# Performance work log

Hardware: AMD Instinct MI355X
Metric: run time of the kernel (lower is better)

The kernel has to match this reference:

```python
import jax, jax.numpy as jnp
import numpy as np

N_EMBD = 1024
N_HEAD = 16
HEAD_SIZE = N_EMBD // N_HEAD


def setup_inputs() -> dict:
    key = jax.random.key(0)
    k_x, k_w, k_b = jax.random.split(key, 3)
    B, T, C = 2, 2048, N_EMBD
    x = jax.random.normal(k_x, (B, T, C), dtype=jnp.float32)
    # Linear(n_embd, 3*n_embd): weight [C, 3C] (applied as x @ W), bias [3C]
    w_qkv = jax.random.normal(k_w, (C, 3 * C), dtype=jnp.float32) * (1.0 / np.sqrt(C))
    b_qkv = jax.random.normal(k_b, (3 * C,), dtype=jnp.float32) * 0.02
    return {"x": x, "w_qkv": w_qkv, "b_qkv": b_qkv}


def reference(x, w_qkv, b_qkv):
    B, T, C = x.shape
    H, D = N_HEAD, HEAD_SIZE
    qkv = x @ w_qkv + b_qkv                      # [B, T, 3C]
    q, k, v = jnp.split(qkv, 3, axis=-1)         # each [B, T, C]
    # [B, T, C] -> [B, H, T, D]
    q = q.reshape(B, T, H, D).transpose(0, 2, 1, 3)
    k = k.reshape(B, T, H, D).transpose(0, 2, 1, 3)
    v = v.reshape(B, T, H, D).transpose(0, 2, 1, 3)
    scores = jnp.einsum('bhqd,bhkd->bhqk', q, k) / jnp.sqrt(jnp.float32(D))
    causal = jnp.tril(jnp.ones((T, T), dtype=bool))  # allow j <= i
    scores = jnp.where(causal[None, None, :, :], scores, -jnp.inf)
    weights = jax.nn.softmax(scores, axis=-1)    # [B, H, T, T]
    out = jnp.einsum('bhqk,bhkd->bhqd', weights, v)
    out = out.transpose(0, 2, 1, 3).reshape(B, T, C)
    return out
```

## Files before the change

### kernel.cpp

```cpp
#include <hip/hip_runtime.h>
#include <hip/hip_bf16.h>


#define CDIM  1024
#define C3    3072
#define HS    64
#define TLEN  2048
#define KVT   64
#define KSTR  72
#define VSTR  72
#define SCL   0.1803368801111204f

typedef __attribute__((ext_vector_type(8))) short bf16x8;
typedef __attribute__((ext_vector_type(4))) float f32x4;
typedef __attribute__((ext_vector_type(4))) unsigned short u16x4;

__device__ __forceinline__ unsigned short f2b(float f) {
    unsigned u = __float_as_uint(f);
    unsigned r = (u + 0x7FFFu + ((u >> 16) & 1u)) >> 16;
    return (unsigned short)r;
}
__device__ __forceinline__ float b2f(unsigned short u) {
    return __uint_as_float(((unsigned)u) << 16);
}
__device__ __forceinline__ float fexp2(float x) {
    return __builtin_amdgcn_exp2f(x);
}
__device__ __forceinline__ unsigned pkbf(float a, float b) {
    float2 f; f.x = a; f.y = b;
    __hip_bfloat162 h = __float22bfloat162_rn(f);
    union { __hip_bfloat162 h2; unsigned u; } c;
    c.h2 = h;
    return c.u;
}
__device__ __forceinline__ void gl_lds16(const unsigned short* g, unsigned short* l) {
    __builtin_amdgcn_global_load_lds((const __attribute__((address_space(1))) void*)g,
                                     (__attribute__((address_space(3))) void*)l, 16, 0, 0);
}
__device__ __forceinline__ int detect_bf(const void* bias, int lane) {
    unsigned w = ((const unsigned*)bias)[lane];
    unsigned e = (w >> 7) & 0xFF;
    unsigned long long m = __ballot(e >= 100 && e <= 135);
    return __popcll(m) >= 48;
}

__device__ __forceinline__ void plswap(unsigned x, unsigned& y0, unsigned& y1) {
    unsigned aa = x, bb = x;
    asm("v_permlane32_swap_b32 %0, %1" : "+v"(aa), "+v"(bb));
    asm("v_permlane16_swap_b32 %0, %1" : "+v"(aa), "+v"(bb));
    y0 = aa; y1 = bb;
}
__device__ __forceinline__ bf16x8 xfrag(unsigned x00, unsigned x01,
                                        unsigned x10, unsigned x11, int qsel) {
    unsigned y000, y100, y001, y101, y010, y110, y011, y111;
    plswap(x00, y000, y100);
    plswap(x01, y001, y101);
    plswap(x10, y010, y110);
    plswap(x11, y011, y111);
    union { unsigned u[4]; bf16x8 v; } r;
    r.u[0] = qsel ? y010 : y000;
    r.u[1] = qsel ? y011 : y001;
    r.u[2] = qsel ? y110 : y100;
    r.u[3] = qsel ? y111 : y101;
    return r.v;
}

__global__ __launch_bounds__(256) void k_prep(const void* __restrict__ w,
                                              const void* __restrict__ x,
                                              const void* __restrict__ bias,
                                              unsigned short* __restrict__ wt,
                                              unsigned short* __restrict__ xb) {
    __shared__ unsigned short tile[64 * 66];
    int t = threadIdx.x;
    int isbf = detect_bf(bias, t & 63);
    int bid = blockIdx.x;

    if (bid < 768) {
        int n0 = (bid % 48) * 64;
        int k0 = (bid / 48) * 64;
        for (int i = 0; i < 16; ++i) {
            int idx = t + i * 256;
            int r = idx >> 6, c = idx & 63;
            unsigned short v;
            if (isbf) v = ((const unsigned short*)w)[(k0 + r) * C3 + n0 + c];
            else      v = f2b(((const float*)w)[(k0 + r) * C3 + n0 + c]);
            tile[r * 66 + c] = v;
        }
        __syncthreads();
        for (int i = 0; i < 16; ++i) {
            int idx = t + i * 256;
            int r = idx >> 6, c = idx & 63;
            wt[(n0 + r) * CDIM + k0 + c] = tile[c * 66 + r];
        }
    }
    if (!isbf) {
        const float* s = (const float*)x;
        unsigned* d = (unsigned*)xb;
        int base = bid * 1024;
        for (int j = t; j < 1024; j += 256) {
            int idx = base + j;
            float a = s[2 * idx], b = s[2 * idx + 1];
            d[idx] = (unsigned)f2b(a) | ((unsigned)f2b(b) << 16);
        }
    }
}

__global__ __launch_bounds__(256, 3) void k_gemm_qkv(const void* __restrict__ xraw,
                                                     const unsigned short* __restrict__ xb,
                                                     const void* __restrict__ biasraw,
                                                     const unsigned short* __restrict__ Bt,
                                                     unsigned short* __restrict__ qk,
                                                     unsigned short* __restrict__ vtg) {
    __shared__ __align__(16) unsigned short As[128 * 64];
    __shared__ __align__(16) unsigned short Bs[128 * 64];
    int tid  = threadIdx.x;
    int lane = tid & 63, wv = tid >> 6;
    int quad = lane >> 4, l16 = lane & 15;
    int isbf = detect_bf(biasraw, lane);
    const unsigned short* A = isbf ? (const unsigned short*)xraw : xb;

    int lin = blockIdx.x + 24 * blockIdx.y;
    int swz = (lin & 7) * 96 + (lin >> 3);
    int m0 = (swz / 24) * 128, n0 = (swz % 24) * 128;
    int wm = (wv >> 1) * 64, wn = (wv & 1) * 64;

    f32x4 acc[4][4] = {};

    int srow = wv * 8 + (lane >> 3);
    int kcg8 = (((lane & 7) ^ (lane >> 3)) * 8);
    const unsigned short* Ag = A  + (m0 + srow) * CDIM + kcg8;
    const unsigned short* Bg = Bt + (n0 + srow) * CDIM + kcg8;
    unsigned short* lA = &As[srow * 64 + (lane & 7) * 8];
    unsigned short* lB = &Bs[srow * 64 + (lane & 7) * 8];

    for (int k0 = 0; k0 < CDIM; k0 += 64) {
        __syncthreads();
        for (int j = 0; j < 4; ++j) {
            gl_lds16(Ag + j * (32 * CDIM), lA + j * (32 * 64));
            gl_lds16(Bg + j * (32 * CDIM), lB + j * (32 * 64));
        }
        Ag += 64; Bg += 64;
        __syncthreads();

        for (int kk = 0; kk < 2; ++kk) {
            int sw = (l16 & 7);
            bf16x8 af[4], bfr[4];
            for (int mt = 0; mt < 4; ++mt)
                af[mt] = *(const bf16x8*)&As[(wm + mt * 16 + l16) * 64 + (((kk * 4 + quad) ^ sw) * 8)];
            for (int nt = 0; nt < 4; ++nt)
                bfr[nt] = *(const bf16x8*)&Bs[(wn + nt * 16 + l16) * 64 + (((kk * 4 + quad) ^ sw) * 8)];
            for (int mt = 0; mt < 4; ++mt)
                for (int nt = 0; nt < 4; ++nt)
                    acc[mt][nt] = __builtin_amdgcn_mfma_f32_16x16x32_bf16(af[mt], bfr[nt], acc[mt][nt], 0, 0, 0);
        }
    }

    if (n0 < 2048) {
        for (int mt = 0; mt < 4; ++mt) {
            int row = m0 + wm + mt * 16 + quad * 4;
            for (int nt = 0; nt < 4; ++nt) {
                int col = n0 + wn + nt * 16 + l16;
                float bv = isbf ? b2f(((const unsigned short*)biasraw)[col])
                                : ((const float*)biasraw)[col];
                for (int i = 0; i < 4; ++i)
                    qk[(row + i) * 2048 + col] = f2b(acc[mt][nt][i] + bv);
            }
        }
    } else {
        for (int mt = 0; mt < 4; ++mt) {
            int row = m0 + wm + mt * 16 + quad * 4;
            int t = row & 2047, b = row >> 11;
            for (int nt = 0; nt < 4; ++nt) {
                int col = n0 + wn + nt * 16 + l16;
                float bv = isbf ? b2f(((const unsigned short*)biasraw)[col])
                                : ((const float*)biasraw)[col];
                int hh = (col - 2048) >> 6, d = (col - 2048) & 63;
                u16x4 pk;
                for (int i = 0; i < 4; ++i) pk[i] = f2b(acc[mt][nt][i] + bv);
                *(u16x4*)&vtg[((b * 16 + hh) * 64 + d) * TLEN + t] = pk;
            }
        }
    }
}

__global__ __launch_bounds__(256, 4) void k_attn(const unsigned short* __restrict__ qk,
                                                 const unsigned short* __restrict__ vtg,
                                                 const void* __restrict__ biasraw,
                                                 void* __restrict__ outv) {
    __shared__ __align__(16) unsigned short SM[2 * 64 * KSTR];
    unsigned short* Ks = SM;
    unsigned short* Vt = SM + 64 * KSTR;

    int tid  = threadIdx.x;
    int lane = tid & 63, wv = tid >> 6;
    int quad = lane >> 4, l16 = lane & 15;
    int isbf = detect_bf(biasraw, lane);
    int bh = blockIdx.x;
    int g  = 31 - blockIdx.y;
    int b = bh >> 4, h = bh & 15;
    int rowbase = b * TLEN;

    int s_ = wv >> 1;
    int p  = wv & 1;
    int qbase = 64 * g + 32 * s_;
    int T = g + 1;

    bf16x8 qf[2][2];
    for (int qt = 0; qt < 2; ++qt)
        for (int kh = 0; kh < 2; ++kh)
            qf[qt][kh] = *(const bf16x8*)&qk[(rowbase + qbase + qt * 16 + l16) * 2048
                                            + h * HS + kh * 32 + quad * 8];

    f32x4 o[2][4] = {};
    float ls[2] = {0.f, 0.f};

    int srow = tid >> 2;
    int sc   = (tid & 3) * 8;
    const unsigned short* kgB = qk  + (rowbase + srow) * 2048 + CDIM + h * HS + sc;
    const unsigned short* vgB = vtg + (bh * 64 + srow) * TLEN + sc;

    {
        uint4 k0 = *(const uint4*)kgB;
        uint4 k1 = *(const uint4*)(kgB + 32);
        uint4 v0 = *(const uint4*)vgB;
        uint4 v1 = *(const uint4*)(vgB + 32);
        *(uint4*)&Ks[srow * KSTR + sc]      = k0;
        *(uint4*)&Ks[srow * KSTR + sc + 32] = k1;
        *(uint4*)&Vt[srow * VSTR + sc]      = v0;
        *(uint4*)&Vt[srow * VSTR + sc + 32] = v1;
    }
    const unsigned short* kpf = kgB + KVT * 2048;
    const unsigned short* vpf = vgB + KVT;
    __syncthreads();

    for (int t = 0; t < T; ++t) {
        int kv0 = t * KVT;
        bool act = (p == 0) || (s_ == 1) || (t < T - 1);
        bool dm  = (t == T - 1) && (p == s_);

        uint4 kn0, kn1, vn0, vn1;
        bool pf = (t + 1 < T);
        if (pf) {
            kn0 = *(const uint4*)kpf;
            kn1 = *(const uint4*)(kpf + 32);
            vn0 = *(const uint4*)vpf;
            vn1 = *(const uint4*)(vpf + 32);
            kpf += KVT * 2048;
            vpf += KVT;
        }

        unsigned sp[2][2][2];
        if (act) {
            bf16x8 kf[2][2];
            #pragma unroll
            for (int nt = 0; nt < 2; ++nt) {
                const unsigned short* kb = &Ks[(32 * p + nt * 16 + l16) * KSTR + quad * 8];
                kf[nt][0] = *(const bf16x8*)kb;
                kf[nt][1] = *(const bf16x8*)(kb + 32);
            }
            f32x4 sv[2][2];
            __builtin_amdgcn_s_setprio(1);
            #pragma unroll
            for (int qt = 0; qt < 2; ++qt)
                #pragma unroll
                for (int nt = 0; nt < 2; ++nt) {
                    f32x4 z = {};
                    z = __builtin_amdgcn_mfma_f32_16x16x32_bf16(kf[nt][0], qf[qt][0], z, 0, 0, 0);
                    z = __builtin_amdgcn_mfma_f32_16x16x32_bf16(kf[nt][1], qf[qt][1], z, 0, 0, 0);
                    sv[qt][nt] = z;
                }
            __builtin_amdgcn_s_setprio(0);
            #pragma unroll
            for (int qt = 0; qt < 2; ++qt) {
                float psum = 0.f;
                int q = qbase + qt * 16 + l16;
                #pragma unroll
                for (int nt = 0; nt < 2; ++nt) {
                    float pv[4];
                    #pragma unroll
                    for (int i = 0; i < 4; ++i) {
                        float arg = fminf(fmaf(sv[qt][nt][i], SCL, -12.0f), 30.0f);
                        if (dm) {
                            int kv = kv0 + 32 * p + nt * 16 + quad * 4 + i;
                            if (kv > q) arg = -1e30f;
                        }
                        pv[i] = fexp2(arg);
                        psum += pv[i];
                    }
                    sp[qt][nt][0] = pkbf(pv[0], pv[1]);
                    sp[qt][nt][1] = pkbf(pv[2], pv[3]);
                }
                ls[qt] += psum;
            }
            int qsel = quad & 2;
            bf16x8 f0 = xfrag(sp[0][0][0], sp[0][0][1], sp[0][1][0], sp[0][1][1], qsel);
            bf16x8 f1 = xfrag(sp[1][0][0], sp[1][0][1], sp[1][1][0], sp[1][1][1], qsel);
            __builtin_amdgcn_s_setprio(1);
            #pragma unroll
            for (int dt = 0; dt < 4; ++dt) {
                bf16x8 av = *(const bf16x8*)&Vt[(dt * 16 + l16) * VSTR + 32 * p + quad * 8];
                o[0][dt] = __builtin_amdgcn_mfma_f32_16x16x32_bf16(av, f0, o[0][dt], 0, 0, 0);
                o[1][dt] = __builtin_amdgcn_mfma_f32_16x16x32_bf16(av, f1, o[1][dt], 0, 0, 0);
            }
            __builtin_amdgcn_s_setprio(0);
        }

        __syncthreads();
        if (pf) {
            *(uint4*)&Ks[srow * KSTR + sc]      = kn0;
            *(uint4*)&Ks[srow * KSTR + sc + 32] = kn1;
            *(uint4*)&Vt[srow * VSTR + sc]      = vn0;
            *(uint4*)&Vt[srow * VSTR + sc + 32] = vn1;
        }
        __syncthreads();
    }

    #pragma unroll
    for (int qt = 0; qt < 2; ++qt) {
        ls[qt] += __shfl_xor(ls[qt], 16);
        ls[qt] += __shfl_xor(ls[qt], 32);
    }
    float* mrg  = (float*)SM;
    float* lbuf = (float*)SM + 4352;

    if (p == 1) {
        #pragma unroll
        for (int qt = 0; qt < 2; ++qt)
            #pragma unroll
            for (int dt = 0; dt < 4; ++dt)
                *(f32x4*)&mrg[s_ * (32 * 68) + (qt * 16 + l16) * 68 + dt * 16 + quad * 4] = o[qt][dt];
        if (quad == 0) {
            lbuf[s_ * 32 + l16]      = ls[0];
            lbuf[s_ * 32 + 16 + l16] = ls[1];
        }
    }
    __syncthreads();
    if (p == 0) {
        #pragma unroll
        for (int qt = 0; qt < 2; ++qt) {
            float lt = ls[qt] + lbuf[s_ * 32 + qt * 16 + l16];
            float inv = 1.0f / lt;
            int q = qbase + qt * 16 + l16;
            if (isbf) {
                unsigned short* out = (unsigned short*)outv;
                #pragma unroll
                for (int dt = 0; dt < 4; ++dt) {
                    f32x4 m = *(const f32x4*)&mrg[s_ * (32 * 68) + (qt * 16 + l16) * 68 + dt * 16 + quad * 4];
                    u16x4 ov;
                    #pragma unroll
                    for (int i = 0; i < 4; ++i) ov[i] = f2b((o[qt][dt][i] + m[i]) * inv);
                    *(u16x4*)&out[(rowbase + q) * CDIM + h * HS + dt * 16 + quad * 4] = ov;
                }
            } else {
                float* out = (float*)outv;
                #pragma unroll
                for (int dt = 0; dt < 4; ++dt) {
                    f32x4 m = *(const f32x4*)&mrg[s_ * (32 * 68) + (qt * 16 + l16) * 68 + dt * 16 + quad * 4];
                    float4 ov;
                    ov.x = (o[qt][dt][0] + m[0]) * inv;
                    ov.y = (o[qt][dt][1] + m[1]) * inv;
                    ov.z = (o[qt][dt][2] + m[2]) * inv;
                    ov.w = (o[qt][dt][3] + m[3]) * inv;
                    *(float4*)&out[(rowbase + q) * CDIM + h * HS + dt * 16 + quad * 4] = ov;
                }
            }
        }
    }
}

extern "C" void kernel_launch(void* const* d_in, const int* in_sizes, int n_in,
                              void* d_out, int out_size, void* d_ws, size_t ws_size,
                              hipStream_t stream) {
    const void* x    = d_in[0];
    const void* w    = d_in[1];
    const void* bias = d_in[2];

    char* ws = (char*)d_ws;
    unsigned short* xb  = (unsigned short*)ws;
    unsigned short* wt  = (unsigned short*)(ws + (8u  << 20));
    unsigned short* qk  = (unsigned short*)(ws + (16u << 20));
    unsigned short* vtg = (unsigned short*)(ws + (32u << 20));

    k_prep<<<2048, 256, 0, stream>>>(w, x, bias, wt, xb);
    k_gemm_qkv<<<dim3(24, 32), 256, 0, stream>>>(x, xb, bias, wt, qk, vtg);
    k_attn<<<dim3(32, 32), 256, 0, stream>>>(qk, vtg, bias, d_out);
}
```

Baseline: 150.6 us.

## Load K/V fragments directly from global into registers, drop LDS staging and barriers

The attention kernel no longer stages K and V tiles through shared memory with two block barriers per iteration. Each wave now loads its own MFMA K and V^T fragments straight from global memory into registers, with a one-tile register prefetch for K. Waves with no work on the final tile get a shorter loop, and the causal-mask branch is split out so the common path skips the mask test. The trade is losing cross-wave data sharing: K/V reads are replicated per wave, and the global accesses are uncoalesced and rely on cache hits, in exchange for removing the barrier stalls.

```diff
diff --git a/kernel.cpp b/kernel.cpp
--- a/kernel.cpp
+++ b/kernel.cpp
@@ -7,8 +7,6 @@
 #define HS    64
 #define TLEN  2048
 #define KVT   64
-#define KSTR  72
-#define VSTR  72
 #define SCL   0.1803368801111204f
 
 typedef __attribute__((ext_vector_type(8))) short bf16x8;
@@ -187,9 +185,7 @@
                                                  const unsigned short* __restrict__ vtg,
                                                  const void* __restrict__ biasraw,
                                                  void* __restrict__ outv) {
-    __shared__ __align__(16) unsigned short SM[2 * 64 * KSTR];
-    unsigned short* Ks = SM;
-    unsigned short* Vt = SM + 64 * KSTR;
+    __shared__ __align__(16) float SMf[4416];
 
     int tid  = threadIdx.x;
     int lane = tid & 63, wv = tid >> 6;
@@ -203,7 +199,9 @@
     int s_ = wv >> 1;
     int p  = wv & 1;
     int qbase = 64 * g + 32 * s_;
-    int T = g + 1;
+    int T  = g + 1;
+    int Tw = T - ((s_ == 0 && p == 1) ? 1 : 0);
+    bool dmw = (p == s_);
 
     bf16x8 qf[2][2];
     for (int qt = 0; qt < 2; ++qt)
@@ -214,62 +212,54 @@
     f32x4 o[2][4] = {};
     float ls[2] = {0.f, 0.f};
 
-    int srow = tid >> 2;
-    int sc   = (tid & 3) * 8;
-    const unsigned short* kgB = qk  + (rowbase + srow) * 2048 + CDIM + h * HS + sc;
-    const unsigned short* vgB = vtg + (bh * 64 + srow) * TLEN + sc;
-
-    {
-        uint4 k0 = *(const uint4*)kgB;
-        uint4 k1 = *(const uint4*)(kgB + 32);
-        uint4 v0 = *(const uint4*)vgB;
-        uint4 v1 = *(const uint4*)(vgB + 32);
-        *(uint4*)&Ks[srow * KSTR + sc]      = k0;
-        *(uint4*)&Ks[srow * KSTR + sc + 32] = k1;
-        *(uint4*)&Vt[srow * VSTR + sc]      = v0;
-        *(uint4*)&Vt[srow * VSTR + sc + 32] = v1;
-    }
-    const unsigned short* kpf = kgB + KVT * 2048;
-    const unsigned short* vpf = vgB + KVT;
-    __syncthreads();
-
-    for (int t = 0; t < T; ++t) {
-        int kv0 = t * KVT;
-        bool act = (p == 0) || (s_ == 1) || (t < T - 1);
-        bool dm  = (t == T - 1) && (p == s_);
-
-        uint4 kn0, kn1, vn0, vn1;
-        bool pf = (t + 1 < T);
+    const unsigned short* kp0 = qk + (rowbase + 32 * p + l16) * 2048 + CDIM + h * HS + quad * 8;
+    const unsigned short* kp1 = kp0 + 16 * 2048;
+    const unsigned short* vpb = vtg + (bh * 64 + l16) * 2048 + 32 * p + quad * 8;
+    const unsigned short* vp0 = vpb;
+    const unsigned short* vp1 = vpb + 16 * 2048;
+    const unsigned short* vp2 = vpb + 32 * 2048;
+    const unsigned short* vp3 = vpb + 48 * 2048;
+
+    bf16x8 kA00, kA01, kA10, kA11;
+    if (Tw > 0) {
+        kA00 = *(const bf16x8*)kp0; kA01 = *(const bf16x8*)(kp0 + 32);
+        kA10 = *(const bf16x8*)kp1; kA11 = *(const bf16x8*)(kp1 + 32);
+        kp0 += KVT * 2048; kp1 += KVT * 2048;
+    }
+
+    for (int t = 0; t < Tw; ++t) {
+        bf16x8 av0 = *(const bf16x8*)vp0;
+        bf16x8 av1 = *(const bf16x8*)vp1;
+        bf16x8 av2 = *(const bf16x8*)vp2;
+        bf16x8 av3 = *(const bf16x8*)vp3;
+        vp0 += KVT; vp1 += KVT; vp2 += KVT; vp3 += KVT;
+
+        f32x4 sv[2][2];
+        __builtin_amdgcn_s_setprio(1);
+        #pragma unroll
+        for (int qt = 0; qt < 2; ++qt) {
+            f32x4 z0 = {};
+            z0 = __builtin_amdgcn_mfma_f32_16x16x32_bf16(kA00, qf[qt][0], z0, 0, 0, 0);
+            z0 = __builtin_amdgcn_mfma_f32_16x16x32_bf16(kA01, qf[qt][1], z0, 0, 0, 0);
+            sv[qt][0] = z0;
+            f32x4 z1 = {};
+            z1 = __builtin_amdgcn_mfma_f32_16x16x32_bf16(kA10, qf[qt][0], z1, 0, 0, 0);
+            z1 = __builtin_amdgcn_mfma_f32_16x16x32_bf16(kA11, qf[qt][1], z1, 0, 0, 0);
+            sv[qt][1] = z1;
+        }
+        __builtin_amdgcn_s_setprio(0);
+
+        bf16x8 kB00, kB01, kB10, kB11;
+        bool pf = (t + 1 < Tw);
         if (pf) {
-            kn0 = *(const uint4*)kpf;
-            kn1 = *(const uint4*)(kpf + 32);
-            vn0 = *(const uint4*)vpf;
-            vn1 = *(const uint4*)(vpf + 32);
-            kpf += KVT * 2048;
-            vpf += KVT;
+            kB00 = *(const bf16x8*)kp0; kB01 = *(const bf16x8*)(kp0 + 32);
+            kB10 = *(const bf16x8*)kp1; kB11 = *(const bf16x8*)(kp1 + 32);
+            kp0 += KVT * 2048; kp1 += KVT * 2048;
         }
 
         unsigned sp[2][2][2];
-        if (act) {
-            bf16x8 kf[2][2];
-            #pragma unroll
-            for (int nt = 0; nt < 2; ++nt) {
-                const unsigned short* kb = &Ks[(32 * p + nt * 16 + l16) * KSTR + quad * 8];
-                kf[nt][0] = *(const bf16x8*)kb;
-                kf[nt][1] = *(const bf16x8*)(kb + 32);
-            }
-            f32x4 sv[2][2];
-            __builtin_amdgcn_s_setprio(1);
-            #pragma unroll
-            for (int qt = 0; qt < 2; ++qt)
-                #pragma unroll
-                for (int nt = 0; nt < 2; ++nt) {
-                    f32x4 z = {};
-                    z = __builtin_amdgcn_mfma_f32_16x16x32_bf16(kf[nt][0], qf[qt][0], z, 0, 0, 0);
-                    z = __builtin_amdgcn_mfma_f32_16x16x32_bf16(kf[nt][1], qf[qt][1], z, 0, 0, 0);
-                    sv[qt][nt] = z;
-                }
-            __builtin_amdgcn_s_setprio(0);
+        int kvb = t * KVT + 32 * p;
+        if (dmw && (t == T - 1)) {
             #pragma unroll
             for (int qt = 0; qt < 2; ++qt) {
                 float psum = 0.f;
@@ -280,10 +270,8 @@
                     #pragma unroll
                     for (int i = 0; i < 4; ++i) {
                         float arg = fminf(fmaf(sv[qt][nt][i], SCL, -12.0f), 30.0f);
-                        if (dm) {
-                            int kv = kv0 + 32 * p + nt * 16 + quad * 4 + i;
-                            if (kv > q) arg = -1e30f;
-                        }
+                        int kv = kvb + nt * 16 + quad * 4 + i;
+                        if (kv > q) arg = -1e30f;
                         pv[i] = fexp2(arg);
                         psum += pv[i];
                     }
@@ -292,27 +280,41 @@
                 }
                 ls[qt] += psum;
             }
-            int qsel = quad & 2;
-            bf16x8 f0 = xfrag(sp[0][0][0], sp[0][0][1], sp[0][1][0], sp[0][1][1], qsel);
-            bf16x8 f1 = xfrag(sp[1][0][0], sp[1][0][1], sp[1][1][0], sp[1][1][1], qsel);
-            __builtin_amdgcn_s_setprio(1);
+        } else {
             #pragma unroll
-            for (int dt = 0; dt < 4; ++dt) {
-                bf16x8 av = *(const bf16x8*)&Vt[(dt * 16 + l16) * VSTR + 32 * p + quad * 8];
-                o[0][dt] = __builtin_amdgcn_mfma_f32_16x16x32_bf16(av, f0, o[0][dt], 0, 0, 0);
-                o[1][dt] = __builtin_amdgcn_mfma_f32_16x16x32_bf16(av, f1, o[1][dt], 0, 0, 0);
-            }
-            __builtin_amdgcn_s_setprio(0);
-        }
-
-        __syncthreads();
-        if (pf) {
-            *(uint4*)&Ks[srow * KSTR + sc]      = kn0;
-            *(uint4*)&Ks[srow * KSTR + sc + 32] = kn1;
-            *(uint4*)&Vt[srow * VSTR + sc]      = vn0;
-            *(uint4*)&Vt[srow * VSTR + sc + 32] = vn1;
-        }
-        __syncthreads();
+            for (int qt = 0; qt < 2; ++qt) {
+                float psum = 0.f;
+                #pragma unroll
+                for (int nt = 0; nt < 2; ++nt) {
+                    float pv[4];
+                    #pragma unroll
+                    for (int i = 0; i < 4; ++i) {
+                        float arg = fminf(fmaf(sv[qt][nt][i], SCL, -12.0f), 30.0f);
+                        pv[i] = fexp2(arg);
+                        psum += pv[i];
+                    }
+                    sp[qt][nt][0] = pkbf(pv[0], pv[1]);
+                    sp[qt][nt][1] = pkbf(pv[2], pv[3]);
+                }
+                ls[qt] += psum;
+            }
+        }
+
+        int qsel = quad & 2;
+        bf16x8 f0 = xfrag(sp[0][0][0], sp[0][0][1], sp[0][1][0], sp[0][1][1], qsel);
+        bf16x8 f1 = xfrag(sp[1][0][0], sp[1][0][1], sp[1][1][0], sp[1][1][1], qsel);
+        __builtin_amdgcn_s_setprio(1);
+        o[0][0] = __builtin_amdgcn_mfma_f32_16x16x32_bf16(av0, f0, o[0][0], 0, 0, 0);
+        o[1][0] = __builtin_amdgcn_mfma_f32_16x16x32_bf16(av0, f1, o[1][0], 0, 0, 0);
+        o[0][1] = __builtin_amdgcn_mfma_f32_16x16x32_bf16(av1, f0, o[0][1], 0, 0, 0);
+        o[1][1] = __builtin_amdgcn_mfma_f32_16x16x32_bf16(av1, f1, o[1][1], 0, 0, 0);
+        o[0][2] = __builtin_amdgcn_mfma_f32_16x16x32_bf16(av2, f0, o[0][2], 0, 0, 0);
+        o[1][2] = __builtin_amdgcn_mfma_f32_16x16x32_bf16(av2, f1, o[1][2], 0, 0, 0);
+        o[0][3] = __builtin_amdgcn_mfma_f32_16x16x32_bf16(av3, f0, o[0][3], 0, 0, 0);
+        o[1][3] = __builtin_amdgcn_mfma_f32_16x16x32_bf16(av3, f1, o[1][3], 0, 0, 0);
+        __builtin_amdgcn_s_setprio(0);
+
+        if (pf) { kA00 = kB00; kA01 = kB01; kA10 = kB10; kA11 = kB11; }
     }
 
     #pragma unroll
@@ -320,8 +322,8 @@
         ls[qt] += __shfl_xor(ls[qt], 16);
         ls[qt] += __shfl_xor(ls[qt], 32);
     }
-    float* mrg  = (float*)SM;
-    float* lbuf = (float*)SM + 4352;
+    float* mrg  = SMf;
+    float* lbuf = SMf + 4352;
 
     if (p == 1) {
         #pragma unroll
```

Result: slower. 185.9 us (+23.4%).
